# Kernel tuning notes

Measured on AMD Instinct MI355X. Metric: run time of the kernel, lower is better.

## Reference

```python
import jax, jax.numpy as jnp
import numpy as np

B, S, H, L, G = 8, 512, 768, 10, 3  # batch, seq len, hidden (bert_output_dim), max mention len, gold slots


def _make_bounds():
    # All spans [s, e] inclusive with 0 <= e - s < L, as MentionScoresHead enumerates.
    bounds = [(s, e) for s in range(S) for e in range(s, min(s + L, S))]
    return np.asarray(bounds, dtype=np.int32)  # [M, 2], M = 5075


def setup_inputs() -> dict:
    key = jax.random.key(0)
    k1, k2, k3, k4 = jax.random.split(key, 4)
    bounds = jnp.asarray(_make_bounds())           # [M, 2]
    M = bounds.shape[0]
    mention_bounds = jnp.broadcast_to(bounds, (B, M, 2))
    bert_output = jax.random.normal(k1, (B, S, H), jnp.float32)
    mention_scores = jax.random.normal(k2, (B, M), jnp.float32)
    # gold spans: pick real candidate spans; gold end is exclusive (code does end -= 1)
    gidx = jax.random.randint(k3, (B, G), 0, M)
    gb = jnp.take(bounds, gidx, axis=0)            # [B, G, 2] inclusive
    gold_mention_bounds = gb.at[:, :, 1].add(1)    # exclusive end, as in dataset format
    gold_mention_bounds_mask = jnp.ones((B, G), dtype=bool)
    gold_entity_local_id = jax.random.randint(k4, (B, G), 0, 100000)
    return dict(
        bert_output=bert_output,
        mention_scores=mention_scores,
        mention_bounds=mention_bounds,
        gold_mention_bounds=gold_mention_bounds,
        gold_mention_bounds_mask=gold_mention_bounds_mask,
        gold_entity_local_id=gold_entity_local_id,
    )


def _span_mean(bert_output, start, end):
    # Mean of bert_output[b, start:end+1, :] via exclusive prefix sums. start/end: [B, M] inclusive.
    Bsz, Ssz, Hsz = bert_output.shape
    csum = jnp.cumsum(bert_output, axis=1)
    csum = jnp.concatenate([jnp.zeros((Bsz, 1, Hsz), bert_output.dtype), csum], axis=1)  # [B, S+1, H]
    b_idx = jnp.arange(Bsz)[:, None]
    seg_sum = csum[b_idx, end + 1] - csum[b_idx, start]          # [B, M, H]
    length = (end - start + 1).astype(bert_output.dtype)[..., None]
    return seg_sum / length


def reference(bert_output, mention_scores, mention_bounds, gold_mention_bounds,
              gold_mention_bounds_mask, gold_entity_local_id):
    Bsz, M, _ = mention_bounds.shape
    Hsz = bert_output.shape[2]
    start = mention_bounds[:, :, 0]
    end = mention_bounds[:, :, 1]

    # get_embedding_mention (method='average_all'): mean-pool tokens in each span.
    mention_embedding = _span_mean(bert_output, start, end)      # [B, M, H]

    # prune_mention: match each candidate span against gold spans (inclusive-end gold).
    g2 = gold_mention_bounds.at[:, :, 1].add(-1)                 # [B, G, 2]
    g2 = jnp.where(gold_mention_bounds_mask[..., None], g2, -1)
    match = ((start[:, :, None] == g2[:, None, :, 0])
             & (end[:, :, None] == g2[:, None, :, 1])
             & (g2[:, None, :, 0] >= 0))                         # [B, M, G]
    matched = match.any(axis=-1)
    Gn = g2.shape[1]
    last = (Gn - 1) - jnp.argmax(match[..., ::-1], axis=-1)      # last matching gold idx
    ids = jnp.take_along_axis(gold_entity_local_id, last, axis=1)
    gold_id_extend = jnp.where(matched, ids, -1)                 # [B, M]

    # Keep mask (scores finite & end >= start): all-true by construction -> plain flatten.
    return (
        mention_embedding.reshape(Bsz * M, Hsz),
        mention_scores.reshape(-1, 1),
        mention_bounds.reshape(-1, 2),
        gold_id_extend.reshape(-1, 1),
    )
```

## Files before the change

### kernel.cpp

```cpp
#include <hip/hip_runtime.h>

#define Bsz 8
#define Ssz 512
#define Hsz 768
#define Lsz 10
#define Gsz 3
#define Msz 5075

__global__ void __launch_bounds__(Hsz)
span_mean_kernel(const float* __restrict__ bert, float* __restrict__ out0) {
    const int bs = blockIdx.x;
    const int b = bs / Ssz;
    const int s = bs - b * Ssz;
    const int h = threadIdx.x;

    const int cnt = (Ssz - s < Lsz) ? (Ssz - s) : Lsz;
    const int corr = (s > 503) ? ((s - 503) * (s - 502)) / 2 : 0;
    const int base = 10 * s - corr;

    const float* __restrict__ row = bert + ((size_t)(b * Ssz + s)) * Hsz + h;
    float* __restrict__ out = out0 + ((size_t)b * Msz + base) * (size_t)Hsz + h;

    float acc = 0.0f;
#pragma unroll
    for (int e = 0; e < Lsz; ++e) {
        if (e >= cnt) break;
        acc += row[(size_t)e * Hsz];
        out[(size_t)e * Hsz] = acc / (float)(e + 1);
    }
}

__global__ void meta_kernel(const float* __restrict__ scores,
                            const int* __restrict__ bounds,
                            const int* __restrict__ gold_bounds,
                            const int* __restrict__ gold_ids,
                            float* __restrict__ out1,
                            float* __restrict__ out2,
                            float* __restrict__ out3) {
    const int i = blockIdx.x * blockDim.x + threadIdx.x;
    const int total = Bsz * Msz;
    if (i >= total) return;

    const int b = i / Msz;

    out1[i] = scores[i];

    const int s = bounds[2 * i];
    const int e = bounds[2 * i + 1];
    out2[2 * i]     = (float)s;
    out2[2 * i + 1] = (float)e;

    int id = -1;
#pragma unroll
    for (int g = 0; g < Gsz; ++g) {
        const int gs = gold_bounds[(b * Gsz + g) * 2];
        const int ge = gold_bounds[(b * Gsz + g) * 2 + 1] - 1;
        if (gs >= 0 && gs == s && ge == e) {
            id = gold_ids[b * Gsz + g];
        }
    }
    out3[i] = (float)id;
}

extern "C" void kernel_launch(void* const* d_in, const int* in_sizes, int n_in,
                              void* d_out, int out_size, void* d_ws, size_t ws_size,
                              hipStream_t stream) {
    const float* bert        = (const float*)d_in[0];
    const float* scores      = (const float*)d_in[1];
    const int*   bounds      = (const int*)d_in[2];
    const int*   gold_bounds = (const int*)d_in[3];
    const int*   gold_ids    = (const int*)d_in[5];

    float* out = (float*)d_out;
    const size_t n0 = (size_t)Bsz * Msz * Hsz;
    const size_t n1 = (size_t)Bsz * Msz;
    const size_t n2 = (size_t)Bsz * Msz * 2;
    float* out0 = out;
    float* out1 = out + n0;
    float* out2 = out + n0 + n1;
    float* out3 = out + n0 + n1 + n2;

    span_mean_kernel<<<Bsz * Ssz, Hsz, 0, stream>>>(bert, out0);

    const int total = Bsz * Msz;
    const int blk = 256;
    meta_kernel<<<(total + blk - 1) / blk, blk, 0, stream>>>(
        scores, bounds, gold_bounds, gold_ids, out1, out2, out3);
}
```

Before: 159.1 us.

## Fuse span-mean and metadata kernels with float4 loads, reciprocals, block swizzle

Merges the span-mean kernel and the metadata kernel into a single launch, with the metadata blocks appended after the span blocks. The span path switches to float4 loads and stores with 192 threads, preloads all ten rows when a span group is full, and multiplies by precomputed reciprocals instead of dividing. Block indices are swizzled so that consecutive blocks land on different batches. The aim is to save one launch and raise memory throughput on a store-bound kernel. Reciprocal multiplication can differ slightly in rounding from true division.

```diff
diff --git a/kernel.cpp b/kernel.cpp
--- a/kernel.cpp
+++ b/kernel.cpp
@@ -7,39 +7,70 @@
 #define Gsz 3
 #define Msz 5075
 
-__global__ void __launch_bounds__(Hsz)
-span_mean_kernel(const float* __restrict__ bert, float* __restrict__ out0) {
-    const int bs = blockIdx.x;
-    const int b = bs / Ssz;
-    const int s = bs - b * Ssz;
-    const int h = threadIdx.x;
+#define H4 (Hsz / 4)
+#define THREADS H4
+#define SPAN_BLOCKS (Bsz * Ssz)
+#define META_TOTAL (Bsz * Msz)
+#define META_BLOCKS ((META_TOTAL + THREADS - 1) / THREADS)
 
-    const int cnt = (Ssz - s < Lsz) ? (Ssz - s) : Lsz;
-    const int corr = (s > 503) ? ((s - 503) * (s - 502)) / 2 : 0;
-    const int base = 10 * s - corr;
+__global__ void __launch_bounds__(THREADS)
+fused_kernel(const float* __restrict__ bert,
+             const float* __restrict__ scores,
+             const int* __restrict__ bounds,
+             const int* __restrict__ gold_bounds,
+             const int* __restrict__ gold_ids,
+             float* __restrict__ out0,
+             float* __restrict__ out1,
+             float* __restrict__ out2,
+             float* __restrict__ out3) {
+    const int bid = blockIdx.x;
 
-    const float* __restrict__ row = bert + ((size_t)(b * Ssz + s)) * Hsz + h;
-    float* __restrict__ out = out0 + ((size_t)b * Msz + base) * (size_t)Hsz + h;
+    if (bid < SPAN_BLOCKS) {
+        const int swz = (bid & 7) * (SPAN_BLOCKS / 8) + (bid >> 3);
+        const int b = swz >> 9;
+        const int s = swz & (Ssz - 1);
 
-    float acc = 0.0f;
+        const int cnt = (Ssz - s < Lsz) ? (Ssz - s) : Lsz;
+        const int corr = (s > 503) ? ((s - 503) * (s - 502)) / 2 : 0;
+        const int base = 10 * s - corr;
+
+        const int h4 = threadIdx.x;
+        const float4* __restrict__ row =
+            (const float4*)(bert + ((size_t)(b * Ssz + s)) * Hsz) + h4;
+        float4* __restrict__ out =
+            (float4*)(out0 + ((size_t)b * Msz + base) * (size_t)Hsz) + h4;
+
+        const float RCP[Lsz] = {1.0f, 0.5f, 1.0f/3.0f, 0.25f, 0.2f,
+                                1.0f/6.0f, 1.0f/7.0f, 0.125f, 1.0f/9.0f, 0.1f};
+
+        if (cnt == Lsz) {
+            float4 v[Lsz];
 #pragma unroll
-    for (int e = 0; e < Lsz; ++e) {
-        if (e >= cnt) break;
-        acc += row[(size_t)e * Hsz];
-        out[(size_t)e * Hsz] = acc / (float)(e + 1);
+            for (int e = 0; e < Lsz; ++e) v[e] = row[(size_t)e * H4];
+            float4 acc = make_float4(0.f, 0.f, 0.f, 0.f);
+#pragma unroll
+            for (int e = 0; e < Lsz; ++e) {
+                acc.x += v[e].x; acc.y += v[e].y;
+                acc.z += v[e].z; acc.w += v[e].w;
+                const float r = RCP[e];
+                out[(size_t)e * H4] =
+                    make_float4(acc.x * r, acc.y * r, acc.z * r, acc.w * r);
+            }
+        } else {
+            float4 acc = make_float4(0.f, 0.f, 0.f, 0.f);
+            for (int e = 0; e < cnt; ++e) {
+                const float4 v = row[(size_t)e * H4];
+                acc.x += v.x; acc.y += v.y; acc.z += v.z; acc.w += v.w;
+                const float r = RCP[e];
+                out[(size_t)e * H4] =
+                    make_float4(acc.x * r, acc.y * r, acc.z * r, acc.w * r);
+            }
+        }
+        return;
     }
-}
 
-__global__ void meta_kernel(const float* __restrict__ scores,
-                            const int* __restrict__ bounds,
-                            const int* __restrict__ gold_bounds,
-                            const int* __restrict__ gold_ids,
-                            float* __restrict__ out1,
-                            float* __restrict__ out2,
-                            float* __restrict__ out3) {
-    const int i = blockIdx.x * blockDim.x + threadIdx.x;
-    const int total = Bsz * Msz;
-    if (i >= total) return;
+    const int i = (bid - SPAN_BLOCKS) * THREADS + threadIdx.x;
+    if (i >= META_TOTAL) return;
 
     const int b = i / Msz;
 
@@ -80,10 +111,6 @@
     float* out2 = out + n0 + n1;
     float* out3 = out + n0 + n1 + n2;
 
-    span_mean_kernel<<<Bsz * Ssz, Hsz, 0, stream>>>(bert, out0);
-
-    const int total = Bsz * Msz;
-    const int blk = 256;
-    meta_kernel<<<(total + blk - 1) / blk, blk, 0, stream>>>(
-        scores, bounds, gold_bounds, gold_ids, out1, out2, out3);
+    fused_kernel<<<SPAN_BLOCKS + META_BLOCKS, THREADS, 0, stream>>>(
+        bert, scores, bounds, gold_bounds, gold_ids, out0, out1, out2, out3);
 }
```

Result: faster. 152.0 us (-4.5%).
